# Optimization experiments

Hardware: AMD Instinct MI355X
Metric: run time of the kernel (lower is better)

## Reference

```python
import jax, jax.numpy as jnp
import numpy as np

HID = 512
HEADS = 8
D = HID // HEADS          # att_size = 64
B = 64                    # number of graphs
L = 1024                  # bonds per graph (equal-length scopes)
SCALE = D ** (-0.5)
EPS = 1e-5


def setup_inputs() -> dict:
    key = jax.random.key(0)
    ks = jax.random.split(key, 9)
    f = lambda k, s, sc=1.0: jax.random.normal(k, s, dtype=jnp.float32) * sc
    edge_attr = f(ks[0], (B * L, HID))
    # contiguous equal-length scopes: (start, length) per graph
    scopes = np.stack([np.arange(B, dtype=np.int64) * L,
                       np.full(B, L, dtype=np.int64)], axis=1)
    return {
        "edge_attr": edge_attr,
        "batch_scopes": jnp.asarray(scopes),
        "Wq": f(ks[1], (HID, HID), 0.03),   # torch Linear weight [out, in]
        "Wk": f(ks[2], (HID, HID), 0.03),
        "Wv": f(ks[3], (HID, HID), 0.03),
        "Wr": f(ks[4], (D, D), 0.1),
        "w_alpha": f(ks[5], (D,)),
        "w_beta": f(ks[6], (D,)),
        "Wo": f(ks[7], (HID, HID), 0.03),
        "bo": jnp.zeros((HID,), jnp.float32),
        "ln_g": jnp.ones((HID,), jnp.float32),
        "ln_b": jnp.zeros((HID,), jnp.float32),
    }


def reference(edge_attr, batch_scopes, Wq, Wk, Wv, Wr, w_alpha, w_beta,
              Wo, bo, ln_g, ln_b):
    # Scopes are contiguous, equal length L -> pad_sequence == reshape
    padded = edge_attr.reshape(B, L, HID)

    def proj(W):  # (B, L, HID) @ W.T -> (B, heads, L, D)
        return jnp.einsum('blh,dh->bld', padded, W).reshape(B, L, HEADS, D).transpose(0, 2, 1, 3)

    b_q = proj(Wq)
    b_k = proj(Wk)
    b_v = proj(Wv)

    # softmax over the head-feature dim (faithful to dim=-1 in torch code)
    alpha = jax.nn.softmax(b_q * w_alpha * SCALE, axis=-1)
    global_q = jnp.sum(alpha * b_q, axis=2)            # (B, heads, D), sum over L

    p = global_q[:, :, None, :] * b_k                  # (B, heads, L, D)
    beta = jax.nn.softmax(p * w_beta * SCALE, axis=-1)
    global_k = jnp.sum(beta * p, axis=2)               # (B, heads, D)

    kv = global_k[:, :, None, :] * b_v                 # (B, heads, L, D)
    kv_out = jnp.einsum('bhld,ed->bhle', kv, Wr)
    att = jax.nn.relu(kv_out + b_q)                    # dropout p=0 (eval)

    att = att.transpose(0, 2, 1, 3).reshape(B, L, HID)
    out = jnp.einsum('blh,oh->blo', att, Wo) + bo

    # LayerNorm over last dim
    mu = jnp.mean(out, axis=-1, keepdims=True)
    var = jnp.mean((out - mu) ** 2, axis=-1, keepdims=True)
    out = (out - mu) * jax.lax.rsqrt(var + EPS) * ln_g + ln_b

    # unpad + concat == flatten for equal-length contiguous scopes
    return out.reshape(B * L, HID)
```

## Files before the change

kernel.cpp:

```cpp
#include <hip/hip_runtime.h>
#include <stdint.h>


#define SCALE_F 0.125f
#define EPSF 1e-5f

typedef __attribute__((ext_vector_type(8))) short short8;
typedef __attribute__((ext_vector_type(4))) float float4v;
typedef unsigned short ushort_t;

__device__ __forceinline__ ushort_t f2bf(float f) {
  uint32_t u = __builtin_bit_cast(uint32_t, f);
  u += 0x7fffu + ((u >> 16) & 1u);
  return (ushort_t)(u >> 16);
}
__device__ __forceinline__ float bf2f(ushort_t s) {
  uint32_t u = ((uint32_t)s) << 16;
  return __builtin_bit_cast(float, u);
}

__device__ __forceinline__ void gload16(const void* g, void* l) {
  __builtin_amdgcn_global_load_lds(
      (__attribute__((address_space(1))) char*)(char*)const_cast<void*>(g),
      (__attribute__((address_space(3))) char*)(char*)l, 16, 0, 0);
}

#define BARR() asm volatile("s_barrier" ::: "memory")
#define LGKM0() do { asm volatile("s_waitcnt lgkmcnt(0)" ::: "memory"); \
                     __builtin_amdgcn_sched_barrier(0); } while (0)

__global__ __launch_bounds__(256) void cvt_x(const float* __restrict__ X,
                                             ushort_t* __restrict__ Xb) {
  const int i = blockIdx.x * 256 + threadIdx.x;
  const float4v* src = (const float4v*)X;
  float4v v0 = src[(size_t)i * 2];
  float4v v1 = src[(size_t)i * 2 + 1];
  short8 o;
#pragma unroll
  for (int j = 0; j < 4; ++j) {
    o[j]     = (short)f2bf(v0[j]);
    o[j + 4] = (short)f2bf(v1[j]);
  }
  ((short8*)Xb)[i] = o;
}

__global__ __launch_bounds__(256) void cvt_w(const float* __restrict__ Wq,
                                             const float* __restrict__ Wk,
                                             const float* __restrict__ Wv,
                                             const float* __restrict__ Wo,
                                             ushort_t* __restrict__ Wqkv,
                                             ushort_t* __restrict__ Wob) {
  const int i = blockIdx.x * 256 + threadIdx.x;
  if (i < 262144)        Wqkv[i] = f2bf(Wq[i]);
  else if (i < 524288)   Wqkv[i] = f2bf(Wk[i - 262144]);
  else if (i < 786432)   Wqkv[i] = f2bf(Wv[i - 524288]);
  else                   Wob[i - 786432] = f2bf(Wo[i - 786432]);
}

__global__ __launch_bounds__(512, 2) void gemm8p(const ushort_t* __restrict__ A,
                                                 const ushort_t* __restrict__ Bm,
                                                 ushort_t* __restrict__ C) {
  __shared__ __align__(16) char ldsA[65536];
  __shared__ __align__(16) char ldsB[65536];
  const int swz = (blockIdx.x & 7) * 192 + (blockIdx.x >> 3);
  const int tm = swz / 6, tn = swz % 6;
  const int row0 = tm * 256, col0 = tn * 256;
  const int tid = threadIdx.x, wid = tid >> 6, lane = tid & 63;
  const int wr = wid >> 2, wc = wid & 3;
  const int lr = lane & 15, lk = lane >> 4;
  const int xr = (lr & 7) << 4;

  auto stageA = [&](int kt, int h) {
    const int slot = (2 * kt + h) & 3;
    const int rowbase = row0 + h * 128;
#pragma unroll
    for (int i = 0; i < 2; ++i) {
      const int o = i * 8192 + wid * 1024 + lane * 16;
      const int r = o >> 7, x = o & 127;
      gload16((const char*)A + (size_t)(rowbase + r) * 1024 + kt * 128 + (x ^ ((r & 7) << 4)),
              ldsA + slot * 16384 + i * 8192 + wid * 1024);
    }
  };
  auto stageB = [&](int kt, int h) {
    const int slot = (2 * kt + h) & 3;
    const int rowbase = col0 + h * 128;
#pragma unroll
    for (int i = 0; i < 2; ++i) {
      const int o = i * 8192 + wid * 1024 + lane * 16;
      const int r = o >> 7, x = o & 127;
      gload16((const char*)Bm + (size_t)(rowbase + r) * 1024 + kt * 128 + (x ^ ((r & 7) << 4)),
              ldsB + slot * 16384 + i * 8192 + wid * 1024);
    }
  };
  auto rdA = [&](int t, int mi, int kk) -> short8 {
    const int slot = (2 * t + wr) & 3;
    return *(const short8*)(ldsA + slot * 16384 + (mi * 16 + lr) * 128 +
                            ((kk * 64 + lk * 16) ^ xr));
  };
  auto rdB = [&](int t, int ni, int kk) -> short8 {
    const int slot = (2 * t + (wc >> 1)) & 3;
    return *(const short8*)(ldsB + slot * 16384 + ((wc & 1) * 64 + ni * 16 + lr) * 128 +
                            ((kk * 64 + lk * 16) ^ xr));
  };

  float4v acc[8][4] = {};

  stageA(0, 0); stageA(0, 1); stageB(0, 0); stageB(0, 1);
  stageA(1, 0); stageA(1, 1); stageB(1, 0);
  asm volatile("s_waitcnt vmcnt(6)" ::: "memory");
  BARR();

#pragma unroll
  for (int t = 0; t < 8; ++t) {
    short8 a0[4][2], a1[4][2], b0[2][2], b1[2][2];
#pragma unroll
    for (int mi = 0; mi < 4; ++mi)
#pragma unroll
      for (int kk = 0; kk < 2; ++kk) a0[mi][kk] = rdA(t, mi, kk);
#pragma unroll
    for (int ni = 0; ni < 2; ++ni)
#pragma unroll
      for (int kk = 0; kk < 2; ++kk) b0[ni][kk] = rdB(t, ni, kk);
    if (t + 1 < 8) stageB(t + 1, 1);
    BARR();
    LGKM0();
    __builtin_amdgcn_s_setprio(1);
#pragma unroll
    for (int kk = 0; kk < 2; ++kk)
#pragma unroll
      for (int mi = 0; mi < 4; ++mi)
#pragma unroll
        for (int ni = 0; ni < 2; ++ni)
          acc[mi][ni] = __builtin_amdgcn_mfma_f32_16x16x32_bf16(a0[mi][kk], b0[ni][kk], acc[mi][ni], 0, 0, 0);
    __builtin_amdgcn_s_setprio(0);
    __builtin_amdgcn_sched_barrier(0);
    BARR();
#pragma unroll
    for (int mi = 0; mi < 4; ++mi)
#pragma unroll
      for (int kk = 0; kk < 2; ++kk) a1[mi][kk] = rdA(t, mi + 4, kk);
#pragma unroll
    for (int ni = 0; ni < 2; ++ni)
#pragma unroll
      for (int kk = 0; kk < 2; ++kk) b1[ni][kk] = rdB(t, ni + 2, kk);
    BARR();
    LGKM0();
    __builtin_amdgcn_s_setprio(1);
#pragma unroll
    for (int kk = 0; kk < 2; ++kk)
#pragma unroll
      for (int mi = 0; mi < 4; ++mi)
#pragma unroll
        for (int ni = 0; ni < 2; ++ni)
          acc[mi][ni + 2] = __builtin_amdgcn_mfma_f32_16x16x32_bf16(a0[mi][kk], b1[ni][kk], acc[mi][ni + 2], 0, 0, 0);
    __builtin_amdgcn_s_setprio(0);
    __builtin_amdgcn_sched_barrier(0);
    BARR();
    if (t + 2 < 8) { stageA(t + 2, 0); stageA(t + 2, 1); }
    __builtin_amdgcn_sched_barrier(0);
    __builtin_amdgcn_s_setprio(1);
#pragma unroll
    for (int kk = 0; kk < 2; ++kk)
#pragma unroll
      for (int mi = 0; mi < 4; ++mi)
#pragma unroll
        for (int ni = 0; ni < 2; ++ni)
          acc[mi + 4][ni] = __builtin_amdgcn_mfma_f32_16x16x32_bf16(a1[mi][kk], b0[ni][kk], acc[mi + 4][ni], 0, 0, 0);
    __builtin_amdgcn_s_setprio(0);
    __builtin_amdgcn_sched_barrier(0);
    BARR();
    if (t + 2 < 8) stageB(t + 2, 0);
    __builtin_amdgcn_sched_barrier(0);
    __builtin_amdgcn_s_setprio(1);
#pragma unroll
    for (int kk = 0; kk < 2; ++kk)
#pragma unroll
      for (int mi = 0; mi < 4; ++mi)
#pragma unroll
        for (int ni = 0; ni < 2; ++ni)
          acc[mi + 4][ni + 2] = __builtin_amdgcn_mfma_f32_16x16x32_bf16(a1[mi][kk], b1[ni][kk], acc[mi + 4][ni + 2], 0, 0, 0);
    __builtin_amdgcn_s_setprio(0);
    __builtin_amdgcn_sched_barrier(0);
    if (t < 6) {
      asm volatile("s_waitcnt vmcnt(6)" ::: "memory");
    } else if (t == 6) {
      asm volatile("s_waitcnt vmcnt(0)" ::: "memory");
    }
    BARR();
  }

#pragma unroll
  for (int mi = 0; mi < 8; ++mi)
#pragma unroll
    for (int ni = 0; ni < 4; ++ni) {
      const int col = col0 + wc * 64 + ni * 16 + lr;
#pragma unroll
      for (int r = 0; r < 4; ++r) {
        const int row = row0 + wr * 128 + mi * 16 + lk * 4 + r;
        C[(size_t)row * 1536 + col] = f2bf(acc[mi][ni][r]);
      }
    }
}

__global__ __launch_bounds__(256) void reduce_gq(const ushort_t* __restrict__ QKV,
                                                 const float* __restrict__ w_alpha,
                                                 float* __restrict__ gq_part) {
  const int bx = blockIdx.x, bh = bx >> 2, ch = bx & 3;
  const int b = bh >> 3, h = bh & 7;
  const int tid = threadIdx.x, wid = tid >> 6, lane = tid & 63;
  const int rsub = lane >> 3, dch = lane & 7;
  __shared__ float red[4][64];
  float wa[8];
#pragma unroll
  for (int j = 0; j < 8; ++j) wa[j] = w_alpha[dch * 8 + j] * SCALE_F;
  const size_t base = (size_t)b * 1024 + ch * 256;
  float acc[8] = {0, 0, 0, 0, 0, 0, 0, 0};
  for (int it = 0; it < 8; ++it) {
    const size_t t = base + it * 32 + wid * 8 + rsub;
    short8 raw = *(const short8*)(QKV + t * 1536 + h * 64 + dch * 8);
    float q[8], s[8];
#pragma unroll
    for (int j = 0; j < 8; ++j) { q[j] = bf2f((ushort_t)raw[j]); s[j] = q[j] * wa[j]; }
    float m = s[0];
#pragma unroll
    for (int j = 1; j < 8; ++j) m = fmaxf(m, s[j]);
    m = fmaxf(m, __shfl_xor(m, 1)); m = fmaxf(m, __shfl_xor(m, 2)); m = fmaxf(m, __shfl_xor(m, 4));
    float e[8], sum = 0.f;
#pragma unroll
    for (int j = 0; j < 8; ++j) { e[j] = __expf(s[j] - m); sum += e[j]; }
    sum += __shfl_xor(sum, 1); sum += __shfl_xor(sum, 2); sum += __shfl_xor(sum, 4);
    const float inv = 1.0f / sum;
#pragma unroll
    for (int j = 0; j < 8; ++j) acc[j] += e[j] * inv * q[j];
  }
#pragma unroll
  for (int msk = 8; msk < 64; msk <<= 1)
#pragma unroll
    for (int j = 0; j < 8; ++j) acc[j] += __shfl_xor(acc[j], msk);
  if (lane < 8) {
#pragma unroll
    for (int j = 0; j < 8; ++j) red[wid][lane * 8 + j] = acc[j];
  }
  __syncthreads();
  if (tid < 64)
    gq_part[(size_t)bx * 64 + tid] = red[0][tid] + red[1][tid] + red[2][tid] + red[3][tid];
}

__global__ __launch_bounds__(256) void reduce_gk(const ushort_t* __restrict__ QKV,
                                                 const float* __restrict__ w_beta,
                                                 const float* __restrict__ gq_part,
                                                 float* __restrict__ gk_part) {
  const int bx = blockIdx.x, bh = bx >> 2, ch = bx & 3;
  const int b = bh >> 3, h = bh & 7;
  const int tid = threadIdx.x, wid = tid >> 6, lane = tid & 63;
  const int rsub = lane >> 3, dch = lane & 7;
  __shared__ float red[4][64];
  __shared__ float gq_s[64];
  if (tid < 64) {
    float s = 0.f;
#pragma unroll
    for (int c = 0; c < 4; ++c) s += gq_part[(size_t)(bh * 4 + c) * 64 + tid];
    gq_s[tid] = s;
  }
  __syncthreads();
  float wb[8], gq[8];
#pragma unroll
  for (int j = 0; j < 8; ++j) {
    wb[j] = w_beta[dch * 8 + j] * SCALE_F;
    gq[j] = gq_s[dch * 8 + j];
  }
  const size_t base = (size_t)b * 1024 + ch * 256;
  float acc[8] = {0, 0, 0, 0, 0, 0, 0, 0};
  for (int it = 0; it < 8; ++it) {
    const size_t t = base + it * 32 + wid * 8 + rsub;
    short8 raw = *(const short8*)(QKV + t * 1536 + 512 + h * 64 + dch * 8);
    float p[8], s[8];
#pragma unroll
    for (int j = 0; j < 8; ++j) { p[j] = gq[j] * bf2f((ushort_t)raw[j]); s[j] = p[j] * wb[j]; }
    float m = s[0];
#pragma unroll
    for (int j = 1; j < 8; ++j) m = fmaxf(m, s[j]);
    m = fmaxf(m, __shfl_xor(m, 1)); m = fmaxf(m, __shfl_xor(m, 2)); m = fmaxf(m, __shfl_xor(m, 4));
    float e[8], sum = 0.f;
#pragma unroll
    for (int j = 0; j < 8; ++j) { e[j] = __expf(s[j] - m); sum += e[j]; }
    sum += __shfl_xor(sum, 1); sum += __shfl_xor(sum, 2); sum += __shfl_xor(sum, 4);
    const float inv = 1.0f / sum;
#pragma unroll
    for (int j = 0; j < 8; ++j) acc[j] += e[j] * inv * p[j];
  }
#pragma unroll
  for (int msk = 8; msk < 64; msk <<= 1)
#pragma unroll
    for (int j = 0; j < 8; ++j) acc[j] += __shfl_xor(acc[j], msk);
  if (lane < 8) {
#pragma unroll
    for (int j = 0; j < 8; ++j) red[wid][lane * 8 + j] = acc[j];
  }
  __syncthreads();
  if (tid < 64)
    gk_part[(size_t)bx * 64 + tid] = red[0][tid] + red[1][tid] + red[2][tid] + red[3][tid];
}

__global__ __launch_bounds__(256) void att_k(const ushort_t* __restrict__ QKV,
                                             const float* __restrict__ Wr,
                                             const float* __restrict__ gk_part,
                                             ushort_t* __restrict__ att) {
  const int bx = blockIdx.x, bh = bx >> 2, tc = bx & 3;
  const int b = bh >> 3, h = bh & 7;
  const int tid = threadIdx.x, wid = tid >> 6, lane = tid & 63;
  __shared__ float gk_s[64];
  __shared__ __align__(16) ushort_t Ml[64 * 72];
  if (tid < 64) {
    float s = 0.f;
#pragma unroll
    for (int c = 0; c < 4; ++c) s += gk_part[(size_t)(bh * 4 + c) * 64 + tid];
    gk_s[tid] = s;
  }
  __syncthreads();
  for (int i = tid; i < 4096; i += 256) {
    const int e = i >> 6, d = i & 63;
    Ml[e * 72 + d] = f2bf(Wr[i] * gk_s[d]);
  }
  __syncthreads();
  const int lr = lane & 15, lk = lane >> 4;
  short8 bfr[4][2], bfi[4][2];
#pragma unroll
  for (int ni = 0; ni < 4; ++ni)
#pragma unroll
    for (int ks = 0; ks < 2; ++ks) {
      bfr[ni][ks] = *(const short8*)&Ml[(ni * 16 + lr) * 72 + ks * 32 + lk * 8];
#pragma unroll
      for (int j = 0; j < 8; ++j)
        bfi[ni][ks][j] = (ni * 16 + lr == ks * 32 + lk * 8 + j) ? (short)0x3F80 : (short)0;
    }
  const size_t tw = (size_t)b * 1024 + tc * 256 + wid * 64;
  float4v oacc[4][4] = {};
#pragma unroll
  for (int ks = 0; ks < 2; ++ks) {
    short8 a[4], aq[4];
#pragma unroll
    for (int mi = 0; mi < 4; ++mi) {
      const size_t t = tw + mi * 16 + lr;
      a[mi]  = *(const short8*)(QKV + t * 1536 + 1024 + h * 64 + ks * 32 + lk * 8);
      aq[mi] = *(const short8*)(QKV + t * 1536 +        h * 64 + ks * 32 + lk * 8);
    }
#pragma unroll
    for (int mi = 0; mi < 4; ++mi)
#pragma unroll
      for (int ni = 0; ni < 4; ++ni) {
        oacc[mi][ni] = __builtin_amdgcn_mfma_f32_16x16x32_bf16(a[mi],  bfr[ni][ks], oacc[mi][ni], 0, 0, 0);
        oacc[mi][ni] = __builtin_amdgcn_mfma_f32_16x16x32_bf16(aq[mi], bfi[ni][ks], oacc[mi][ni], 0, 0, 0);
      }
  }
#pragma unroll
  for (int mi = 0; mi < 4; ++mi)
#pragma unroll
    for (int ni = 0; ni < 4; ++ni)
#pragma unroll
      for (int r = 0; r < 4; ++r) {
        const size_t t = tw + mi * 16 + lk * 4 + r;
        const int e = ni * 16 + lr;
        att[t * 512 + h * 64 + e] = f2bf(fmaxf(oacc[mi][ni][r], 0.0f));
      }
}

__global__ __launch_bounds__(512, 2) void gemm_ln(const ushort_t* __restrict__ A,
                                                  const ushort_t* __restrict__ Bm,
                                                  float* __restrict__ out,
                                                  const float* __restrict__ bo,
                                                  const float* __restrict__ lng,
                                                  const float* __restrict__ lnb) {
  __shared__ __align__(16) ushort_t As[2][128 * 32];
  __shared__ __align__(16) ushort_t Bs[2][512 * 32];
  __shared__ float red_s[4][128][2];
  __shared__ float tot_s[128][2];
  const int tid = threadIdx.x, wid = tid >> 6, lane = tid & 63;
  const int wr = wid >> 2, wc = wid & 3;
  const int lr = lane & 15, lk = lane >> 4;
  const int row0 = blockIdx.x * 128;
  float4v acc[4][8] = {};

  const int la = lane * 16;
  const int ar = wid * 16 + (lane >> 2);
  const int acb = (lane & 3) * 16;

  auto stage = [&](int buf, int s) {
    const int k0b = s * 64;
    gload16((const char*)A + (size_t)(row0 + ar) * 1024 + k0b + acb,
            (char*)&As[buf][0] + wid * 1024);
#pragma unroll
    for (int i = 0; i < 4; ++i) {
      const int dst = (wid * 4 + i) * 1024;
      const int br = (dst + la) >> 6;
      const int bcb = la & 63;
      gload16((const char*)Bm + (size_t)br * 1024 + k0b + bcb,
              (char*)&Bs[buf][0] + dst);
    }
  };

  stage(0, 0);
  __syncthreads();
  for (int s = 0; s < 16; ++s) {
    const int buf = s & 1;
    if (s < 15) stage(buf ^ 1, s + 1);
    short8 af[4], bf[8];
#pragma unroll
    for (int mi = 0; mi < 4; ++mi)
      af[mi] = *(const short8*)((const char*)&As[buf][0] + (wr * 64 + mi * 16 + lr) * 64 + lk * 16);
#pragma unroll
    for (int ni = 0; ni < 8; ++ni)
      bf[ni] = *(const short8*)((const char*)&Bs[buf][0] + (wc * 128 + ni * 16 + lr) * 64 + lk * 16);
#pragma unroll
    for (int mi = 0; mi < 4; ++mi)
#pragma unroll
      for (int ni = 0; ni < 8; ++ni)
        acc[mi][ni] = __builtin_amdgcn_mfma_f32_16x16x32_bf16(af[mi], bf[ni], acc[mi][ni], 0, 0, 0);
    __syncthreads();
  }

  float bov[8], gv[8], bv[8];
#pragma unroll
  for (int ni = 0; ni < 8; ++ni) {
    const int c = wc * 128 + ni * 16 + lr;
    bov[ni] = bo[c]; gv[ni] = lng[c]; bv[ni] = lnb[c];
  }
#pragma unroll
  for (int mi = 0; mi < 4; ++mi)
#pragma unroll
    for (int ni = 0; ni < 8; ++ni)
#pragma unroll
      for (int r = 0; r < 4; ++r)
        acc[mi][ni][r] += bov[ni];
#pragma unroll
  for (int mi = 0; mi < 4; ++mi)
#pragma unroll
    for (int r = 0; r < 4; ++r) {
      float s = 0.f, q = 0.f;
#pragma unroll
      for (int ni = 0; ni < 8; ++ni) { const float v = acc[mi][ni][r]; s += v; q += v * v; }
      s += __shfl_xor(s, 1); q += __shfl_xor(q, 1);
      s += __shfl_xor(s, 2); q += __shfl_xor(q, 2);
      s += __shfl_xor(s, 4); q += __shfl_xor(q, 4);
      s += __shfl_xor(s, 8); q += __shfl_xor(q, 8);
      if (lr == 0) {
        const int rb = wr * 64 + mi * 16 + lk * 4 + r;
        red_s[wc][rb][0] = s;
        red_s[wc][rb][1] = q;
      }
    }
  __syncthreads();
  if (tid < 128) {
    tot_s[tid][0] = red_s[0][tid][0] + red_s[1][tid][0] + red_s[2][tid][0] + red_s[3][tid][0];
    tot_s[tid][1] = red_s[0][tid][1] + red_s[1][tid][1] + red_s[2][tid][1] + red_s[3][tid][1];
  }
  __syncthreads();
#pragma unroll
  for (int mi = 0; mi < 4; ++mi)
#pragma unroll
    for (int r = 0; r < 4; ++r) {
      const int rb = wr * 64 + mi * 16 + lk * 4 + r;
      const float mu = tot_s[rb][0] * (1.f / 512.f);
      const float var = tot_s[rb][1] * (1.f / 512.f) - mu * mu;
      const float rs = rsqrtf(var + EPSF);
      float* op = out + (size_t)(row0 + rb) * 512 + wc * 128 + lr;
#pragma unroll
      for (int ni = 0; ni < 8; ++ni)
        op[ni * 16] = (acc[mi][ni][r] - mu) * rs * gv[ni] + bv[ni];
    }
}

extern "C" void kernel_launch(void* const* d_in, const int* in_sizes, int n_in,
                              void* d_out, int out_size, void* d_ws, size_t ws_size,
                              hipStream_t stream) {
  const float* X       = (const float*)d_in[0];
  const float* Wq      = (const float*)d_in[2];
  const float* Wk      = (const float*)d_in[3];
  const float* Wv      = (const float*)d_in[4];
  const float* Wr      = (const float*)d_in[5];
  const float* w_alpha = (const float*)d_in[6];
  const float* w_beta  = (const float*)d_in[7];
  const float* Wo      = (const float*)d_in[8];
  const float* bo      = (const float*)d_in[9];
  const float* ln_g    = (const float*)d_in[10];
  const float* ln_b    = (const float*)d_in[11];

  char* ws = (char*)d_ws;
  ushort_t* Xb      = (ushort_t*)(ws);
  ushort_t* Wqkv    = (ushort_t*)(ws + 67108864);
  ushort_t* Wob     = (ushort_t*)(ws + 68681728);
  ushort_t* QKV     = (ushort_t*)(ws + 69206016);
  float*    gq_part = (float*)(ws + 270532608);
  float*    gk_part = (float*)(ws + 271056896);
  ushort_t* att     = Xb;
  float* out = (float*)d_out;

  hipLaunchKernelGGL(cvt_x, dim3(16384), dim3(256), 0, stream, X, Xb);
  hipLaunchKernelGGL(cvt_w, dim3(4096), dim3(256), 0, stream, Wq, Wk, Wv, Wo, Wqkv, Wob);
  hipLaunchKernelGGL(gemm8p, dim3(1536), dim3(512), 0, stream, Xb, Wqkv, QKV);
  hipLaunchKernelGGL(reduce_gq, dim3(2048), dim3(256), 0, stream, QKV, w_alpha, gq_part);
  hipLaunchKernelGGL(reduce_gk, dim3(2048), dim3(256), 0, stream, QKV, w_beta, gq_part, gk_part);
  hipLaunchKernelGGL(att_k, dim3(2048), dim3(256), 0, stream, QKV, Wr, gk_part, att);
  hipLaunchKernelGGL(gemm_ln, dim3(512), dim3(512), 0, stream,
                     att, Wob, out, bo, ln_g, ln_b);
}
```

Before: 328.8 us.

## Make QKV GEMM persistent per row block, sweeping all column tiles in one pipeline

Replaces the 1536-block tiled QKV GEMM with 256 blocks, each owning a 256-row stripe and streaming all six 256-column tiles through one continuous 48-step double-buffered K pipeline. Full tiles are loaded per stage into two LDS slots instead of four half-tile slots, and the barrier schedule is simplified. The intent is to remove per-tile prologue/epilogue and pipeline fill costs and keep A rows warm. The trade-off is that the epilogue stores now sit inside the main loop, and the grid relies on exactly one block per CU.

```diff
diff --git a/kernel.cpp b/kernel.cpp
--- a/kernel.cpp
+++ b/kernel.cpp
@@ -25,8 +25,9 @@
       (__attribute__((address_space(3))) char*)(char*)l, 16, 0, 0);
 }
 
-#define BARR() asm volatile("s_barrier" ::: "memory")
-#define LGKM0() do { asm volatile("s_waitcnt lgkmcnt(0)" ::: "memory"); \
+#define SBAR() __builtin_amdgcn_s_barrier()
+#define LGKM0() do { __builtin_amdgcn_sched_barrier(0);                 \
+                     asm volatile("s_waitcnt lgkmcnt(0)" ::: "memory"); \
                      __builtin_amdgcn_sched_barrier(0); } while (0)
 
 __global__ __launch_bounds__(256) void cvt_x(const float* __restrict__ X,
@@ -57,149 +58,117 @@
   else                   Wob[i - 786432] = f2bf(Wo[i - 786432]);
 }
 
-__global__ __launch_bounds__(512, 2) void gemm8p(const ushort_t* __restrict__ A,
-                                                 const ushort_t* __restrict__ Bm,
-                                                 ushort_t* __restrict__ C) {
+__global__ __launch_bounds__(512, 2) void gemm_qkv(const ushort_t* __restrict__ A,
+                                                   const ushort_t* __restrict__ Bm,
+                                                   ushort_t* __restrict__ C) {
   __shared__ __align__(16) char ldsA[65536];
   __shared__ __align__(16) char ldsB[65536];
-  const int swz = (blockIdx.x & 7) * 192 + (blockIdx.x >> 3);
-  const int tm = swz / 6, tn = swz % 6;
-  const int row0 = tm * 256, col0 = tn * 256;
+  const int tm = blockIdx.x;
+  const int row0 = tm * 256;
   const int tid = threadIdx.x, wid = tid >> 6, lane = tid & 63;
   const int wr = wid >> 2, wc = wid & 3;
   const int lr = lane & 15, lk = lane >> 4;
   const int xr = (lr & 7) << 4;
 
-  auto stageA = [&](int kt, int h) {
-    const int slot = (2 * kt + h) & 3;
-    const int rowbase = row0 + h * 128;
-#pragma unroll
-    for (int i = 0; i < 2; ++i) {
+  auto stageA = [&](int s) {
+    const int kt = s & 7;
+#pragma unroll
+    for (int i = 0; i < 4; ++i) {
       const int o = i * 8192 + wid * 1024 + lane * 16;
       const int r = o >> 7, x = o & 127;
-      gload16((const char*)A + (size_t)(rowbase + r) * 1024 + kt * 128 + (x ^ ((r & 7) << 4)),
-              ldsA + slot * 16384 + i * 8192 + wid * 1024);
+      gload16((const char*)A + (size_t)(row0 + r) * 1024 + kt * 128 + (x ^ ((r & 7) << 4)),
+              ldsA + (s & 1) * 32768 + i * 8192 + wid * 1024);
     }
   };
-  auto stageB = [&](int kt, int h) {
-    const int slot = (2 * kt + h) & 3;
-    const int rowbase = col0 + h * 128;
-#pragma unroll
-    for (int i = 0; i < 2; ++i) {
+  auto stageB = [&](int s) {
+    const int kt = s & 7, colb = (s >> 3) * 256;
+#pragma unroll
+    for (int i = 0; i < 4; ++i) {
       const int o = i * 8192 + wid * 1024 + lane * 16;
       const int r = o >> 7, x = o & 127;
-      gload16((const char*)Bm + (size_t)(rowbase + r) * 1024 + kt * 128 + (x ^ ((r & 7) << 4)),
-              ldsB + slot * 16384 + i * 8192 + wid * 1024);
+      gload16((const char*)Bm + (size_t)(colb + r) * 1024 + kt * 128 + (x ^ ((r & 7) << 4)),
+              ldsB + (s & 1) * 32768 + i * 8192 + wid * 1024);
     }
   };
-  auto rdA = [&](int t, int mi, int kk) -> short8 {
-    const int slot = (2 * t + wr) & 3;
-    return *(const short8*)(ldsA + slot * 16384 + (mi * 16 + lr) * 128 +
+  auto rdA = [&](int sl, int mi, int kk) -> short8 {
+    return *(const short8*)(ldsA + sl * 32768 + (wr * 128 + mi * 16 + lr) * 128 +
                             ((kk * 64 + lk * 16) ^ xr));
   };
-  auto rdB = [&](int t, int ni, int kk) -> short8 {
-    const int slot = (2 * t + (wc >> 1)) & 3;
-    return *(const short8*)(ldsB + slot * 16384 + ((wc & 1) * 64 + ni * 16 + lr) * 128 +
+  auto rdB = [&](int sl, int ni, int kk) -> short8 {
+    return *(const short8*)(ldsB + sl * 32768 + (wc * 64 + ni * 16 + lr) * 128 +
                             ((kk * 64 + lk * 16) ^ xr));
   };
 
   float4v acc[8][4] = {};
 
-  stageA(0, 0); stageA(0, 1); stageB(0, 0); stageB(0, 1);
-  stageA(1, 0); stageA(1, 1); stageB(1, 0);
-  asm volatile("s_waitcnt vmcnt(6)" ::: "memory");
-  BARR();
-
-#pragma unroll
-  for (int t = 0; t < 8; ++t) {
-    short8 a0[4][2], a1[4][2], b0[2][2], b1[2][2];
+  stageA(0); stageB(0);
+  stageA(1); stageB(1);
+  asm volatile("s_waitcnt vmcnt(8)" ::: "memory");
+  SBAR();
+
+#pragma unroll 2
+  for (int s = 0; s < 48; ++s) {
+    const int sl = s & 1;
+    short8 a0[4][2], a1[4][2], b[4][2];
 #pragma unroll
     for (int mi = 0; mi < 4; ++mi)
 #pragma unroll
-      for (int kk = 0; kk < 2; ++kk) a0[mi][kk] = rdA(t, mi, kk);
-#pragma unroll
-    for (int ni = 0; ni < 2; ++ni)
-#pragma unroll
-      for (int kk = 0; kk < 2; ++kk) b0[ni][kk] = rdB(t, ni, kk);
-    if (t + 1 < 8) stageB(t + 1, 1);
-    BARR();
+      for (int kk = 0; kk < 2; ++kk) a0[mi][kk] = rdA(sl, mi, kk);
+#pragma unroll
+    for (int ni = 0; ni < 4; ++ni)
+#pragma unroll
+      for (int kk = 0; kk < 2; ++kk) b[ni][kk] = rdB(sl, ni, kk);
     LGKM0();
+    SBAR();
+    if (s + 2 < 48) stageB(s + 2);
+#pragma unroll
+    for (int mi = 0; mi < 4; ++mi)
+#pragma unroll
+      for (int kk = 0; kk < 2; ++kk) a1[mi][kk] = rdA(sl, mi + 4, kk);
     __builtin_amdgcn_s_setprio(1);
 #pragma unroll
     for (int kk = 0; kk < 2; ++kk)
 #pragma unroll
       for (int mi = 0; mi < 4; ++mi)
 #pragma unroll
-        for (int ni = 0; ni < 2; ++ni)
-          acc[mi][ni] = __builtin_amdgcn_mfma_f32_16x16x32_bf16(a0[mi][kk], b0[ni][kk], acc[mi][ni], 0, 0, 0);
+        for (int ni = 0; ni < 4; ++ni)
+          acc[mi][ni] = __builtin_amdgcn_mfma_f32_16x16x32_bf16(a0[mi][kk], b[ni][kk], acc[mi][ni], 0, 0, 0);
+    __builtin_amdgcn_s_setprio(0);
+    LGKM0();
+    SBAR();
+    if (s + 2 < 48) stageA(s + 2);
+    __builtin_amdgcn_s_setprio(1);
+#pragma unroll
+    for (int kk = 0; kk < 2; ++kk)
+#pragma unroll
+      for (int mi = 0; mi < 4; ++mi)
+#pragma unroll
+        for (int ni = 0; ni < 4; ++ni)
+          acc[mi + 4][ni] = __builtin_amdgcn_mfma_f32_16x16x32_bf16(a1[mi][kk], b[ni][kk], acc[mi + 4][ni], 0, 0, 0);
     __builtin_amdgcn_s_setprio(0);
     __builtin_amdgcn_sched_barrier(0);
-    BARR();
-#pragma unroll
-    for (int mi = 0; mi < 4; ++mi)
-#pragma unroll
-      for (int kk = 0; kk < 2; ++kk) a1[mi][kk] = rdA(t, mi + 4, kk);
-#pragma unroll
-    for (int ni = 0; ni < 2; ++ni)
-#pragma unroll
-      for (int kk = 0; kk < 2; ++kk) b1[ni][kk] = rdB(t, ni + 2, kk);
-    BARR();
-    LGKM0();
-    __builtin_amdgcn_s_setprio(1);
-#pragma unroll
-    for (int kk = 0; kk < 2; ++kk)
-#pragma unroll
-      for (int mi = 0; mi < 4; ++mi)
-#pragma unroll
-        for (int ni = 0; ni < 2; ++ni)
-          acc[mi][ni + 2] = __builtin_amdgcn_mfma_f32_16x16x32_bf16(a0[mi][kk], b1[ni][kk], acc[mi][ni + 2], 0, 0, 0);
-    __builtin_amdgcn_s_setprio(0);
-    __builtin_amdgcn_sched_barrier(0);
-    BARR();
-    if (t + 2 < 8) { stageA(t + 2, 0); stageA(t + 2, 1); }
-    __builtin_amdgcn_sched_barrier(0);
-    __builtin_amdgcn_s_setprio(1);
-#pragma unroll
-    for (int kk = 0; kk < 2; ++kk)
-#pragma unroll
-      for (int mi = 0; mi < 4; ++mi)
-#pragma unroll
-        for (int ni = 0; ni < 2; ++ni)
-          acc[mi + 4][ni] = __builtin_amdgcn_mfma_f32_16x16x32_bf16(a1[mi][kk], b0[ni][kk], acc[mi + 4][ni], 0, 0, 0);
-    __builtin_amdgcn_s_setprio(0);
-    __builtin_amdgcn_sched_barrier(0);
-    BARR();
-    if (t + 2 < 8) stageB(t + 2, 0);
-    __builtin_amdgcn_sched_barrier(0);
-    __builtin_amdgcn_s_setprio(1);
-#pragma unroll
-    for (int kk = 0; kk < 2; ++kk)
-#pragma unroll
-      for (int mi = 0; mi < 4; ++mi)
-#pragma unroll
-        for (int ni = 0; ni < 2; ++ni)
-          acc[mi + 4][ni + 2] = __builtin_amdgcn_mfma_f32_16x16x32_bf16(a1[mi][kk], b1[ni][kk], acc[mi + 4][ni + 2], 0, 0, 0);
-    __builtin_amdgcn_s_setprio(0);
-    __builtin_amdgcn_sched_barrier(0);
-    if (t < 6) {
-      asm volatile("s_waitcnt vmcnt(6)" ::: "memory");
-    } else if (t == 6) {
+    if (s < 46) {
+      asm volatile("s_waitcnt vmcnt(8)" ::: "memory");
+    } else if (s == 46) {
       asm volatile("s_waitcnt vmcnt(0)" ::: "memory");
     }
-    BARR();
-  }
-
-#pragma unroll
-  for (int mi = 0; mi < 8; ++mi)
-#pragma unroll
-    for (int ni = 0; ni < 4; ++ni) {
-      const int col = col0 + wc * 64 + ni * 16 + lr;
-#pragma unroll
-      for (int r = 0; r < 4; ++r) {
-        const int row = row0 + wr * 128 + mi * 16 + lk * 4 + r;
-        C[(size_t)row * 1536 + col] = f2bf(acc[mi][ni][r]);
-      }
-    }
+    SBAR();
+    if ((s & 7) == 7) {
+      const int col0 = (s >> 3) * 256;
+#pragma unroll
+      for (int mi = 0; mi < 8; ++mi)
+#pragma unroll
+        for (int ni = 0; ni < 4; ++ni) {
+          const int col = col0 + wc * 64 + ni * 16 + lr;
+#pragma unroll
+          for (int r = 0; r < 4; ++r) {
+            const int row = row0 + wr * 128 + mi * 16 + lk * 4 + r;
+            C[(size_t)row * 1536 + col] = f2bf(acc[mi][ni][r]);
+            acc[mi][ni][r] = 0.0f;
+          }
+        }
+    }
+  }
 }
 
 __global__ __launch_bounds__(256) void reduce_gq(const ushort_t* __restrict__ QKV,
@@ -497,7 +466,7 @@
 
   hipLaunchKernelGGL(cvt_x, dim3(16384), dim3(256), 0, stream, X, Xb);
   hipLaunchKernelGGL(cvt_w, dim3(4096), dim3(256), 0, stream, Wq, Wk, Wv, Wo, Wqkv, Wob);
-  hipLaunchKernelGGL(gemm8p, dim3(1536), dim3(512), 0, stream, Xb, Wqkv, QKV);
+  hipLaunchKernelGGL(gemm_qkv, dim3(256), dim3(512), 0, stream, Xb, Wqkv, QKV);
   hipLaunchKernelGGL(reduce_gq, dim3(2048), dim3(256), 0, stream, QKV, w_alpha, gq_part);
   hipLaunchKernelGGL(reduce_gk, dim3(2048), dim3(256), 0, stream, QKV, w_beta, gq_part, gk_part);
   hipLaunchKernelGGL(att_k, dim3(2048), dim3(256), 0, stream, QKV, Wr, gk_part, att);
```

New measurement: 505.2 us. 53.6% more time.

## Fuse global-query reduction into QKV GEMM epilogue and merge conversion kernels

Applied to the files above, without the earlier changes.

The alpha-softmax weighted sum over L that produces global_q is now computed from the fp32 accumulators in the QKV GEMM epilogue, for the column tiles that hold Q. Each block writes per-wave partials, eight per (batch, head), and the standalone reduce_gq kernel is removed. The X and weight fp32-to-bf16 conversions are merged into one launch. This drops one pass over Q in global memory and two kernel launches, at the cost of a longer GEMM epilogue with many cross-lane shuffles on a third of the tiles.

```diff
diff --git a/kernel.cpp b/kernel.cpp
--- a/kernel.cpp
+++ b/kernel.cpp
@@ -29,37 +29,40 @@
 #define LGKM0() do { asm volatile("s_waitcnt lgkmcnt(0)" ::: "memory"); \
                      __builtin_amdgcn_sched_barrier(0); } while (0)
 
-__global__ __launch_bounds__(256) void cvt_x(const float* __restrict__ X,
-                                             ushort_t* __restrict__ Xb) {
+__global__ __launch_bounds__(256) void cvt_all(const float* __restrict__ X,
+                                               const float* __restrict__ Wq,
+                                               const float* __restrict__ Wk,
+                                               const float* __restrict__ Wv,
+                                               const float* __restrict__ Wo,
+                                               ushort_t* __restrict__ Xb,
+                                               ushort_t* __restrict__ Wqkv,
+                                               ushort_t* __restrict__ Wob) {
   const int i = blockIdx.x * 256 + threadIdx.x;
-  const float4v* src = (const float4v*)X;
-  float4v v0 = src[(size_t)i * 2];
-  float4v v1 = src[(size_t)i * 2 + 1];
-  short8 o;
-#pragma unroll
-  for (int j = 0; j < 4; ++j) {
-    o[j]     = (short)f2bf(v0[j]);
-    o[j + 4] = (short)f2bf(v1[j]);
-  }
-  ((short8*)Xb)[i] = o;
-}
-
-__global__ __launch_bounds__(256) void cvt_w(const float* __restrict__ Wq,
-                                             const float* __restrict__ Wk,
-                                             const float* __restrict__ Wv,
-                                             const float* __restrict__ Wo,
-                                             ushort_t* __restrict__ Wqkv,
-                                             ushort_t* __restrict__ Wob) {
-  const int i = blockIdx.x * 256 + threadIdx.x;
-  if (i < 262144)        Wqkv[i] = f2bf(Wq[i]);
-  else if (i < 524288)   Wqkv[i] = f2bf(Wk[i - 262144]);
-  else if (i < 786432)   Wqkv[i] = f2bf(Wv[i - 524288]);
-  else                   Wob[i - 786432] = f2bf(Wo[i - 786432]);
+  if (i < 4194304) {
+    const float4v* src = (const float4v*)X;
+    float4v v0 = src[(size_t)i * 2];
+    float4v v1 = src[(size_t)i * 2 + 1];
+    short8 o;
+#pragma unroll
+    for (int j = 0; j < 4; ++j) {
+      o[j]     = (short)f2bf(v0[j]);
+      o[j + 4] = (short)f2bf(v1[j]);
+    }
+    ((short8*)Xb)[i] = o;
+  } else {
+    const int j = i - 4194304;
+    if (j < 262144)        Wqkv[j] = f2bf(Wq[j]);
+    else if (j < 524288)   Wqkv[j] = f2bf(Wk[j - 262144]);
+    else if (j < 786432)   Wqkv[j] = f2bf(Wv[j - 524288]);
+    else                   Wob[j - 786432] = f2bf(Wo[j - 786432]);
+  }
 }
 
 __global__ __launch_bounds__(512, 2) void gemm8p(const ushort_t* __restrict__ A,
                                                  const ushort_t* __restrict__ Bm,
-                                                 ushort_t* __restrict__ C) {
+                                                 ushort_t* __restrict__ C,
+                                                 const float* __restrict__ w_alpha,
+                                                 float* __restrict__ gq_part) {
   __shared__ __align__(16) char ldsA[65536];
   __shared__ __align__(16) char ldsB[65536];
   const int swz = (blockIdx.x & 7) * 192 + (blockIdx.x >> 3);
@@ -200,50 +203,44 @@
         C[(size_t)row * 1536 + col] = f2bf(acc[mi][ni][r]);
       }
     }
-}
-
-__global__ __launch_bounds__(256) void reduce_gq(const ushort_t* __restrict__ QKV,
-                                                 const float* __restrict__ w_alpha,
-                                                 float* __restrict__ gq_part) {
-  const int bx = blockIdx.x, bh = bx >> 2, ch = bx & 3;
-  const int b = bh >> 3, h = bh & 7;
-  const int tid = threadIdx.x, wid = tid >> 6, lane = tid & 63;
-  const int rsub = lane >> 3, dch = lane & 7;
-  __shared__ float red[4][64];
-  float wa[8];
-#pragma unroll
-  for (int j = 0; j < 8; ++j) wa[j] = w_alpha[dch * 8 + j] * SCALE_F;
-  const size_t base = (size_t)b * 1024 + ch * 256;
-  float acc[8] = {0, 0, 0, 0, 0, 0, 0, 0};
-  for (int it = 0; it < 8; ++it) {
-    const size_t t = base + it * 32 + wid * 8 + rsub;
-    short8 raw = *(const short8*)(QKV + t * 1536 + h * 64 + dch * 8);
-    float q[8], s[8];
-#pragma unroll
-    for (int j = 0; j < 8; ++j) { q[j] = bf2f((ushort_t)raw[j]); s[j] = q[j] * wa[j]; }
-    float m = s[0];
-#pragma unroll
-    for (int j = 1; j < 8; ++j) m = fmaxf(m, s[j]);
-    m = fmaxf(m, __shfl_xor(m, 1)); m = fmaxf(m, __shfl_xor(m, 2)); m = fmaxf(m, __shfl_xor(m, 4));
-    float e[8], sum = 0.f;
-#pragma unroll
-    for (int j = 0; j < 8; ++j) { e[j] = __expf(s[j] - m); sum += e[j]; }
-    sum += __shfl_xor(sum, 1); sum += __shfl_xor(sum, 2); sum += __shfl_xor(sum, 4);
-    const float inv = 1.0f / sum;
-#pragma unroll
-    for (int j = 0; j < 8; ++j) acc[j] += e[j] * inv * q[j];
-  }
-#pragma unroll
-  for (int msk = 8; msk < 64; msk <<= 1)
-#pragma unroll
-    for (int j = 0; j < 8; ++j) acc[j] += __shfl_xor(acc[j], msk);
-  if (lane < 8) {
-#pragma unroll
-    for (int j = 0; j < 8; ++j) red[wid][lane * 8 + j] = acc[j];
-  }
-  __syncthreads();
-  if (tid < 64)
-    gq_part[(size_t)bx * 64 + tid] = red[0][tid] + red[1][tid] + red[2][tid] + red[3][tid];
+
+  if (tn < 2) {
+    float wa[4];
+#pragma unroll
+    for (int ni = 0; ni < 4; ++ni) wa[ni] = w_alpha[ni * 16 + lr] * SCALE_F;
+    float gqa[4] = {0.f, 0.f, 0.f, 0.f};
+#pragma unroll
+    for (int mi = 0; mi < 8; ++mi)
+#pragma unroll
+      for (int r = 0; r < 4; ++r) {
+        float sv[4];
+#pragma unroll
+        for (int ni = 0; ni < 4; ++ni) sv[ni] = acc[mi][ni][r] * wa[ni];
+        float mx = fmaxf(fmaxf(sv[0], sv[1]), fmaxf(sv[2], sv[3]));
+        mx = fmaxf(mx, __shfl_xor(mx, 1)); mx = fmaxf(mx, __shfl_xor(mx, 2));
+        mx = fmaxf(mx, __shfl_xor(mx, 4)); mx = fmaxf(mx, __shfl_xor(mx, 8));
+        float e[4], sm = 0.f;
+#pragma unroll
+        for (int ni = 0; ni < 4; ++ni) { e[ni] = __expf(sv[ni] - mx); sm += e[ni]; }
+        sm += __shfl_xor(sm, 1); sm += __shfl_xor(sm, 2);
+        sm += __shfl_xor(sm, 4); sm += __shfl_xor(sm, 8);
+        const float inv = 1.0f / sm;
+#pragma unroll
+        for (int ni = 0; ni < 4; ++ni) gqa[ni] += e[ni] * inv * acc[mi][ni][r];
+      }
+#pragma unroll
+    for (int ni = 0; ni < 4; ++ni) {
+      gqa[ni] += __shfl_xor(gqa[ni], 16);
+      gqa[ni] += __shfl_xor(gqa[ni], 32);
+    }
+    if (lk == 0) {
+      const int bh = (tm >> 2) * 8 + tn * 4 + wc;
+      const int sub = (tm & 3) * 2 + wr;
+#pragma unroll
+      for (int ni = 0; ni < 4; ++ni)
+        gq_part[((size_t)bh * 8 + sub) * 64 + ni * 16 + lr] = gqa[ni];
+    }
+  }
 }
 
 __global__ __launch_bounds__(256) void reduce_gk(const ushort_t* __restrict__ QKV,
@@ -259,7 +256,7 @@
   if (tid < 64) {
     float s = 0.f;
 #pragma unroll
-    for (int c = 0; c < 4; ++c) s += gq_part[(size_t)(bh * 4 + c) * 64 + tid];
+    for (int c = 0; c < 8; ++c) s += gq_part[((size_t)bh * 8 + c) * 64 + tid];
     gq_s[tid] = s;
   }
   __syncthreads();
@@ -491,15 +488,16 @@
   ushort_t* Wob     = (ushort_t*)(ws + 68681728);
   ushort_t* QKV     = (ushort_t*)(ws + 69206016);
   float*    gq_part = (float*)(ws + 270532608);
-  float*    gk_part = (float*)(ws + 271056896);
+  float*    gk_part = (float*)(ws + 271581184);
   ushort_t* att     = Xb;
   float* out = (float*)d_out;
 
-  hipLaunchKernelGGL(cvt_x, dim3(16384), dim3(256), 0, stream, X, Xb);
-  hipLaunchKernelGGL(cvt_w, dim3(4096), dim3(256), 0, stream, Wq, Wk, Wv, Wo, Wqkv, Wob);
-  hipLaunchKernelGGL(gemm8p, dim3(1536), dim3(512), 0, stream, Xb, Wqkv, QKV);
-  hipLaunchKernelGGL(reduce_gq, dim3(2048), dim3(256), 0, stream, QKV, w_alpha, gq_part);
-  hipLaunchKernelGGL(reduce_gk, dim3(2048), dim3(256), 0, stream, QKV, w_beta, gq_part, gk_part);
+  hipLaunchKernelGGL(cvt_all, dim3(20480), dim3(256), 0, stream,
+                     X, Wq, Wk, Wv, Wo, Xb, Wqkv, Wob);
+  hipLaunchKernelGGL(gemm8p, dim3(1536), dim3(512), 0, stream,
+                     Xb, Wqkv, QKV, w_alpha, gq_part);
+  hipLaunchKernelGGL(reduce_gk, dim3(2048), dim3(256), 0, stream,
+                     QKV, w_beta, gq_part, gk_part);
   hipLaunchKernelGGL(att_k, dim3(2048), dim3(256), 0, stream, QKV, Wr, gk_part, att);
   hipLaunchKernelGGL(gemm_ln, dim3(512), dim3(512), 0, stream,
                      att, Wob, out, bo, ln_g, ln_b);
```

Result: slower. 347.8 us (+5.8%).
